# Kernel optimization log

Hardware: AMD Instinct MI355X
Metric: run time of the kernel (lower is better)

Reference implementation:

```python
import jax, jax.numpy as jnp
import numpy as np

# Dims: B=batch, H=query heads, HKV=kv heads, T=query len, S=cache/key len, Dh=head dim
B, H, HKV, T, S, Dh = 2, 32, 8, 1024, 2048, 128
THRESH = 0.000488  # keep keys whose mean attention (over heads and queries) exceeds this


def setup_inputs() -> dict:
    key = jax.random.key(0)
    k1, k2, k3 = jax.random.split(key, 3)
    # attn_w emulates post-softmax attention probabilities: rows sum to 1 over key axis
    attn_w = jax.random.uniform(k1, (B, H, T, S), dtype=jnp.float32)
    attn_w = attn_w / attn_w.sum(axis=-1, keepdims=True)
    v = jax.random.normal(k2, (B, HKV, S, Dh), dtype=jnp.float32)
    w_o = jax.random.normal(k3, (H * Dh, H * Dh), dtype=jnp.float32) * 0.02  # o_proj weight (no bias, Mistral)
    return {"attn_w": attn_w, "v": v, "w_o": w_o}


def reference(attn_w, v, w_o):
    # keep = attn_w.mean(dim=(1,2)) > thresh  -> [B, S]
    keep = attn_w.mean(axis=(1, 2)) > THRESH
    pruned_weights = attn_w * keep[:, None, None, :].astype(attn_w.dtype)  # [B,H,T,S]
    # repeat_kv: [B,HKV,S,Dh] -> [B,H,S,Dh] via repeat_interleave on head axis
    groups = attn_w.shape[1] // v.shape[1]
    v_full = jnp.repeat(v, groups, axis=1)
    new_ctx = jnp.einsum('bhts,bhsd->bhtd', pruned_weights, v_full)  # [B,H,T,Dh]
    Bn, Hn, Tn, Dn = new_ctx.shape
    new_ctx = new_ctx.transpose(0, 2, 1, 3).reshape(Bn, Tn, Hn * Dn)  # [B,T,H*Dh]
    out = new_ctx @ w_o.T  # o_proj
    return (out, pruned_weights)
```

## Files before the change

kernel.cpp:

```cpp
#include <hip/hip_runtime.h>
#include <hip/hip_bf16.h>

#define B_ 2
#define H_ 32
#define HKV_ 8
#define T_ 1024
#define S_ 2048
#define DH_ 128
#define HD_ 4096
#define NROW_ 32768
#define THRESH_D 0.000488

typedef __attribute__((ext_vector_type(4))) float f32x4;
typedef __attribute__((ext_vector_type(8))) short bf16x8;

#define SCHED0() __builtin_amdgcn_sched_barrier(0)

__device__ __forceinline__ void gload_lds16(const void* g, void* l) {
  __builtin_amdgcn_global_load_lds(
      (const __attribute__((address_space(1))) void*)g,
      (__attribute__((address_space(3))) void*)l, 16, 0, 0);
}

__global__ __launch_bounds__(256) void colsum_partial_k(
    const float* __restrict__ attn, double* __restrict__ partial) {
  int tid = threadIdx.x;
  int b = blockIdx.z, y = blockIdx.y;
  int s = blockIdx.x * 1024 + tid * 4;
  const float* base = attn + (size_t)(b * NROW_ + y * 128) * S_ + s;
  double a0 = 0.0, a1 = 0.0, a2 = 0.0, a3 = 0.0;
  for (int r = 0; r < 128; ++r) {
    f32x4 vv = *(const f32x4*)(base + (size_t)r * S_);
    a0 += vv.x; a1 += vv.y; a2 += vv.z; a3 += vv.w;
  }
  double* o = partial + (size_t)(b * 256 + y) * S_ + s;
  o[0] = a0; o[1] = a1; o[2] = a2; o[3] = a3;
}

__global__ void reduce_keep_k(const double* __restrict__ partial,
                              float* __restrict__ keep) {
  __shared__ double sh[4][64];
  int b = blockIdx.x >> 5;
  int s0 = (blockIdx.x & 31) * 64;
  int w = threadIdx.x >> 6, l = threadIdx.x & 63;
  const double* p = partial + (size_t)b * 256 * S_ + s0 + l;
  double sum = 0.0;
  #pragma unroll 8
  for (int y = 0; y < 64; ++y) sum += p[(size_t)(w * 64 + y) * S_];
  sh[w][l] = sum;
  __syncthreads();
  if (w == 0) {
    double t = (sh[0][l] + sh[1][l]) + (sh[2][l] + sh[3][l]);
    keep[b * S_ + s0 + l] = (t * (1.0 / 32768.0) > THRESH_D) ? 1.0f : 0.0f;
  }
}

__global__ void convert_v_k(const float* __restrict__ v,
                            __hip_bfloat16* __restrict__ vt) {
  __shared__ float tile[32][33];
  int bh = blockIdx.z;
  int s0 = blockIdx.x * 32, d0 = blockIdx.y * 32;
  const float* vp = v + (size_t)bh * (S_ * DH_);
  __hip_bfloat16* vtp = vt + (size_t)bh * (S_ * DH_);
  int tx = threadIdx.x, ty = threadIdx.y;
  for (int i = 0; i < 32; i += 8)
    tile[ty + i][tx] = vp[(size_t)(s0 + ty + i) * DH_ + d0 + tx];
  __syncthreads();
  int s = s0 + tx;
  for (int i = 0; i < 32; i += 8) {
    int d = d0 + ty + i;
    int ssw = (s & ~63) | ((s ^ ((d & 7) << 3)) & 63);
    vtp[(size_t)d * S_ + ssw] = __float2bfloat16(tile[tx][ty + i]);
  }
}

__global__ void convert_wo_k(const float* __restrict__ w,
                             __hip_bfloat16* __restrict__ wb) {
  size_t idx = ((size_t)blockIdx.x * 256 + threadIdx.x) * 8;
  int n = (int)(idx >> 12);
  int k0 = (int)(idx & (HD_ - 1));
  float4 x = *(const float4*)(w + idx);
  float4 y = *(const float4*)(w + idx + 4);
  union { bf16x8 v8; __hip_bfloat16 h[8]; } u;
  u.h[0] = __float2bfloat16(x.x); u.h[1] = __float2bfloat16(x.y);
  u.h[2] = __float2bfloat16(x.z); u.h[3] = __float2bfloat16(x.w);
  u.h[4] = __float2bfloat16(y.x); u.h[5] = __float2bfloat16(y.y);
  u.h[6] = __float2bfloat16(y.z); u.h[7] = __float2bfloat16(y.w);
  int ksw = (k0 & ~63) | ((k0 ^ ((n & 7) << 3)) & 63);
  *(bf16x8*)(wb + (size_t)n * HD_ + ksw) = u.v8;
}

#define BK1 64
#define NS1 32

__global__ __launch_bounds__(512, 4) void prune_gemm1_k(
    const float* __restrict__ attn, const float* __restrict__ keep,
    const __hip_bfloat16* __restrict__ vt, float* __restrict__ pruned,
    __hip_bfloat16* __restrict__ ctx) {
  __shared__ __align__(16) __hip_bfloat16 As[2][128 * BK1];
  __shared__ __align__(16) __hip_bfloat16 Bs[2][128 * BK1];
  __shared__ __align__(16) float ksh[S_];

  int tid = threadIdx.x;
  int lg = ((blockIdx.x & 7) << 6) | (blockIdx.x >> 3);
  int bh = lg >> 3;
  int t0 = (lg & 7) * 128;
  int b = bh >> 5, h = bh & 31, hkv = h >> 2;
  int rot = (lg * 17) & 31;
  const float* A = attn + ((size_t)bh * T_ + t0) * S_;
  float* P = pruned + ((size_t)bh * T_ + t0) * S_;
  const __hip_bfloat16* Bv = vt + (size_t)(b * HKV_ + hkv) * (DH_ * S_);
  const float* kp = keep + b * S_;

  int arow = tid >> 2;
  int acol = (tid & 3) * 16;
  int wave = tid >> 6, lane = tid & 63;
  int l16 = lane & 15, lk = lane >> 4;

  f32x4 acc[8];
  f32x4 z = {0.f, 0.f, 0.f, 0.f};
  #pragma unroll
  for (int n = 0; n < 8; ++n) acc[n] = z;

  f32x4 areg0[4], areg1[4];

  auto col = [&](int j) { return (j + rot) & 31; };

  auto issueA = [&](int cks, f32x4* bank) {
    const float* ga = A + (size_t)arow * S_ + cks * BK1 + acol;
    #pragma unroll
    for (int j = 0; j < 4; ++j) bank[j] = *(const f32x4*)(ga + j * 4);
  };

  auto issueB = [&](int cks, int buf) {
    const __hip_bfloat16* g0 = Bv + (size_t)(tid >> 3) * S_ + cks * BK1 + (tid & 7) * 8;
    char* lb = (char*)&Bs[buf][0] + tid * 16;
    gload_lds16(g0, lb);
    gload_lds16(g0 + (size_t)64 * S_, lb + 8192);
  };

  auto stageA = [&](int cks, int buf, const f32x4* bank) {
    f32x4 p[4];
    #pragma unroll
    for (int j = 0; j < 4; ++j) {
      f32x4 kv = *(const f32x4*)&ksh[cks * BK1 + acol + j * 4];
      p[j] = bank[j] * kv;
    }
    float* gp = P + (size_t)arow * S_ + cks * BK1 + acol;
    #pragma unroll
    for (int j = 0; j < 4; ++j) *(f32x4*)(gp + j * 4) = p[j];
    union { bf16x8 v8; __hip_bfloat16 h[8]; } u0, u1;
    const float* pf = (const float*)&p[0];
    #pragma unroll
    for (int j = 0; j < 8; ++j) u0.h[j] = __float2bfloat16(pf[j]);
    #pragma unroll
    for (int j = 0; j < 8; ++j) u1.h[j] = __float2bfloat16(pf[8 + j]);
    char* ab = (char*)&As[buf][0];
    int base0 = arow * 128 + acol * 2;
    int sw = (arow & 7) << 4;
    *(bf16x8*)(ab + (base0 ^ sw)) = u0.v8;
    *(bf16x8*)(ab + ((base0 + 16) ^ sw)) = u1.v8;
  };

  auto mfmaStep = [&](int buf) {
    char* ab = (char*)&As[buf][0];
    char* bb = (char*)&Bs[buf][0];
    #pragma unroll
    for (int kk = 0; kk < 2; ++kk) {
      int kb = kk * 64 + lk * 16;
      int ar = wave * 16 + l16;
      bf16x8 af = *(const bf16x8*)(ab + (ar * 128 + (kb ^ ((ar & 7) << 4))));
      #pragma unroll
      for (int n = 0; n < 8; ++n) {
        int br = n * 16 + l16;
        bf16x8 bf = *(const bf16x8*)(bb + (br * 128 + (kb ^ ((br & 7) << 4))));
        acc[n] = __builtin_amdgcn_mfma_f32_16x16x32_bf16(af, bf, acc[n], 0, 0, 0);
      }
    }
  };

  gload_lds16(kp + tid * 4, (char*)ksh + tid * 16);
  issueB(col(0), 0);
  issueA(col(0), areg0);
  SCHED0();
  asm volatile("s_waitcnt vmcnt(6)" ::: "memory");
  SCHED0();
  __builtin_amdgcn_s_barrier();
  SCHED0();
  issueA(col(1), areg1);
  stageA(col(0), 0, areg0);

  for (int ks = 0; ks < NS1; ks += 2) {
    {
      int cur = 0;
      if (ks + 1 < NS1) issueB(col(ks + 1), 1);
      if (ks + 2 < NS1) issueA(col(ks + 2), areg0);
      if (ks + 1 < NS1) stageA(col(ks + 1), 1, areg1);
      SCHED0();
      if (ks + 2 < NS1)      { asm volatile("s_waitcnt vmcnt(18) lgkmcnt(0)" ::: "memory"); }
      else if (ks + 1 < NS1) { asm volatile("s_waitcnt vmcnt(14) lgkmcnt(0)" ::: "memory"); }
      else                   { asm volatile("s_waitcnt vmcnt(4) lgkmcnt(0)" ::: "memory"); }
      SCHED0();
      __builtin_amdgcn_s_barrier();
      SCHED0();
      mfmaStep(cur);
      SCHED0();
      __builtin_amdgcn_s_barrier();
      SCHED0();
    }
    {
      int ko = ks + 1;
      int cur = 1;
      if (ko + 1 < NS1) issueB(col(ko + 1), 0);
      if (ko + 2 < NS1) issueA(col(ko + 2), areg1);
      if (ko + 1 < NS1) stageA(col(ko + 1), 0, areg0);
      SCHED0();
      if (ko + 2 < NS1)      { asm volatile("s_waitcnt vmcnt(18) lgkmcnt(0)" ::: "memory"); }
      else if (ko + 1 < NS1) { asm volatile("s_waitcnt vmcnt(14) lgkmcnt(0)" ::: "memory"); }
      else                   { asm volatile("s_waitcnt vmcnt(4) lgkmcnt(0)" ::: "memory"); }
      SCHED0();
      __builtin_amdgcn_s_barrier();
      SCHED0();
      mfmaStep(cur);
      SCHED0();
      __builtin_amdgcn_s_barrier();
      SCHED0();
    }
  }

  #pragma unroll
  for (int n = 0; n < 8; ++n)
    #pragma unroll
    for (int r = 0; r < 4; ++r) {
      int trow = t0 + wave * 16 + lk * 4 + r;
      int rowm = b * T_ + trow;
      int kcol = h * DH_ + n * 16 + l16;
      int ksw = (kcol & ~63) | ((kcol ^ ((rowm & 7) << 3)) & 63);
      ctx[(size_t)rowm * HD_ + ksw] = __float2bfloat16(acc[n][r]);
    }
}

#define BK2 64
#define NS2 64

__global__ __launch_bounds__(512) void gemm2_k(
    const __hip_bfloat16* __restrict__ Actx,
    const __hip_bfloat16* __restrict__ Bw,
    float* __restrict__ out) {
  __shared__ __align__(16) __hip_bfloat16 As[2][128 * BK2];
  __shared__ __align__(16) __hip_bfloat16 Bs[2][128 * BK2];
  int tid = threadIdx.x;
  int lg = ((blockIdx.x & 7) << 6) | (blockIdx.x >> 3);
  int n0 = (lg >> 4) * 128;
  int m0 = (lg & 15) * 128;
  const __hip_bfloat16* Ap = Actx + (size_t)m0 * HD_;
  const __hip_bfloat16* Bp = Bw + (size_t)n0 * HD_;
  int wave = tid >> 6, lane = tid & 63;
  int l16 = lane & 15, lk = lane >> 4;

  f32x4 acc[8];
  f32x4 z = {0.f, 0.f, 0.f, 0.f};
  #pragma unroll
  for (int n = 0; n < 8; ++n) acc[n] = z;

  auto issue = [&](int ks, int buf) {
    const __hip_bfloat16* ga = Ap + (size_t)(tid >> 3) * HD_ + ks * BK2 + (tid & 7) * 8;
    const __hip_bfloat16* gb = Bp + (size_t)(tid >> 3) * HD_ + ks * BK2 + (tid & 7) * 8;
    char* la = (char*)&As[buf][0] + tid * 16;
    char* lb = (char*)&Bs[buf][0] + tid * 16;
    gload_lds16(ga, la);
    gload_lds16(ga + (size_t)64 * HD_, la + 8192);
    gload_lds16(gb, lb);
    gload_lds16(gb + (size_t)64 * HD_, lb + 8192);
  };

  auto mfmaStep = [&](int buf) {
    char* ab = (char*)&As[buf][0];
    char* bb = (char*)&Bs[buf][0];
    #pragma unroll
    for (int kk = 0; kk < 2; ++kk) {
      int kb = kk * 64 + lk * 16;
      int ar = wave * 16 + l16;
      bf16x8 af = *(const bf16x8*)(ab + (ar * 128 + (kb ^ ((ar & 7) << 4))));
      #pragma unroll
      for (int n = 0; n < 8; ++n) {
        int br = n * 16 + l16;
        bf16x8 bf = *(const bf16x8*)(bb + (br * 128 + (kb ^ ((br & 7) << 4))));
        acc[n] = __builtin_amdgcn_mfma_f32_16x16x32_bf16(af, bf, acc[n], 0, 0, 0);
      }
    }
  };

  issue(0, 0);
  for (int ks = 0; ks < NS2; ++ks) {
    int cur = ks & 1;
    if (ks + 1 < NS2) issue(ks + 1, cur ^ 1);
    SCHED0();
    if (ks + 1 < NS2) {
      asm volatile("s_waitcnt vmcnt(4) lgkmcnt(0)" ::: "memory");
    } else {
      asm volatile("s_waitcnt vmcnt(0) lgkmcnt(0)" ::: "memory");
    }
    SCHED0();
    __builtin_amdgcn_s_barrier();
    SCHED0();
    mfmaStep(cur);
    SCHED0();
    __builtin_amdgcn_s_barrier();
    SCHED0();
  }

  #pragma unroll
  for (int n = 0; n < 8; ++n)
    #pragma unroll
    for (int r = 0; r < 4; ++r) {
      int row = m0 + wave * 16 + lk * 4 + r;
      int col = n0 + n * 16 + l16;
      out[(size_t)row * HD_ + col] = acc[n][r];
    }
}

extern "C" void kernel_launch(void* const* d_in, const int* in_sizes, int n_in,
                              void* d_out, int out_size, void* d_ws, size_t ws_size,
                              hipStream_t stream) {
  const float* attn = (const float*)d_in[0];
  const float* v = (const float*)d_in[1];
  const float* w_o = (const float*)d_in[2];
  float* out = (float*)d_out;
  float* pruned = out + (size_t)B_ * T_ * HD_;

  char* ws = (char*)d_ws;
  size_t off = 0;
  double* partial = (double*)(ws + off); off += (size_t)B_ * 256 * S_ * 8;
  float* keep = (float*)(ws + off);      off += (size_t)B_ * S_ * 4;
  __hip_bfloat16* vt = (__hip_bfloat16*)(ws + off);
  off += (size_t)B_ * HKV_ * DH_ * S_ * 2;
  __hip_bfloat16* wo = (__hip_bfloat16*)(ws + off);
  off += (size_t)HD_ * HD_ * 2;
  __hip_bfloat16* ctx = (__hip_bfloat16*)(ws + off);
  off += (size_t)B_ * T_ * HD_ * 2;

  colsum_partial_k<<<dim3(2, 256, B_), 256, 0, stream>>>(attn, partial);
  reduce_keep_k<<<dim3(64), 256, 0, stream>>>(partial, keep);
  convert_v_k<<<dim3(S_ / 32, DH_ / 32, B_ * HKV_), dim3(32, 8), 0, stream>>>(v, vt);
  convert_wo_k<<<dim3((HD_ * HD_) / (256 * 8)), 256, 0, stream>>>(w_o, wo);
  prune_gemm1_k<<<dim3(512), 512, 0, stream>>>(attn, keep, vt, pruned, ctx);
  gemm2_k<<<dim3(512), 512, 0, stream>>>(ctx, wo, out);

  (void)in_sizes; (void)n_in; (void)out_size; (void)ws_size;
}
```

Measured before the change: 473.9 us.

## Emit bf16 copy of attention during column-sum and feed GEMM1 from it

The column-sum pass now also writes a swizzled bf16 copy of the attention weights. The prune+GEMM1 kernel then streams that half-size copy instead of the fp32 input, and rebuilds the fp32 pruned output from the bf16 values times the keep mask. The keep mask is also folded into the bf16 V conversion. Total DRAM traffic is roughly unchanged, because the extra bf16 write offsets the smaller read, and the pruned-weights output is now rounded to bf16, which risks accuracy. The path only runs when the workspace is large enough to hold the copy; otherwise the old kernels run.

```diff
diff --git a/kernel.cpp b/kernel.cpp
--- a/kernel.cpp
+++ b/kernel.cpp
@@ -22,20 +22,6 @@
       (__attribute__((address_space(3))) void*)l, 16, 0, 0);
 }
 
-__global__ __launch_bounds__(256) void colsum_partial_k(
-    const float* __restrict__ attn, double* __restrict__ partial) {
-  int tid = threadIdx.x;
-  int b = blockIdx.z, y = blockIdx.y;
-  int s = blockIdx.x * 1024 + tid * 4;
-  const float* base = attn + (size_t)(b * NROW_ + y * 128) * S_ + s;
-  double a0 = 0.0, a1 = 0.0, a2 = 0.0, a3 = 0.0;
-  for (int r = 0; r < 128; ++r) {
-    f32x4 vv = *(const f32x4*)(base + (size_t)r * S_);
-    a0 += vv.x; a1 += vv.y; a2 += vv.z; a3 += vv.w;
-  }
-  double* o = partial + (size_t)(b * 256 + y) * S_ + s;
-  o[0] = a0; o[1] = a1; o[2] = a2; o[3] = a3;
-}
 
 __global__ void reduce_keep_k(const double* __restrict__ partial,
                               float* __restrict__ keep) {
@@ -55,8 +41,304 @@
   }
 }
 
-__global__ void convert_v_k(const float* __restrict__ v,
-                            __hip_bfloat16* __restrict__ vt) {
+__global__ void convert_wo_k(const float* __restrict__ w,
+                             __hip_bfloat16* __restrict__ wb) {
+  size_t idx = ((size_t)blockIdx.x * 256 + threadIdx.x) * 8;
+  int n = (int)(idx >> 12);
+  int k0 = (int)(idx & (HD_ - 1));
+  float4 x = *(const float4*)(w + idx);
+  float4 y = *(const float4*)(w + idx + 4);
+  union { bf16x8 v8; __hip_bfloat16 h[8]; } u;
+  u.h[0] = __float2bfloat16(x.x); u.h[1] = __float2bfloat16(x.y);
+  u.h[2] = __float2bfloat16(x.z); u.h[3] = __float2bfloat16(x.w);
+  u.h[4] = __float2bfloat16(y.x); u.h[5] = __float2bfloat16(y.y);
+  u.h[6] = __float2bfloat16(y.z); u.h[7] = __float2bfloat16(y.w);
+  int ksw = (k0 & ~63) | ((k0 ^ ((n & 7) << 3)) & 63);
+  *(bf16x8*)(wb + (size_t)n * HD_ + ksw) = u.v8;
+}
+
+#define BK2 64
+#define NS2 64
+
+__global__ __launch_bounds__(512) void gemm2_k(
+    const __hip_bfloat16* __restrict__ Actx,
+    const __hip_bfloat16* __restrict__ Bw,
+    float* __restrict__ out) {
+  __shared__ __align__(16) __hip_bfloat16 As[2][128 * BK2];
+  __shared__ __align__(16) __hip_bfloat16 Bs[2][128 * BK2];
+  int tid = threadIdx.x;
+  int lg = ((blockIdx.x & 7) << 6) | (blockIdx.x >> 3);
+  int n0 = (lg >> 4) * 128;
+  int m0 = (lg & 15) * 128;
+  const __hip_bfloat16* Ap = Actx + (size_t)m0 * HD_;
+  const __hip_bfloat16* Bp = Bw + (size_t)n0 * HD_;
+  int wave = tid >> 6, lane = tid & 63;
+  int l16 = lane & 15, lk = lane >> 4;
+
+  f32x4 acc[8];
+  f32x4 z = {0.f, 0.f, 0.f, 0.f};
+  #pragma unroll
+  for (int n = 0; n < 8; ++n) acc[n] = z;
+
+  auto issue = [&](int ks, int buf) {
+    const __hip_bfloat16* ga = Ap + (size_t)(tid >> 3) * HD_ + ks * BK2 + (tid & 7) * 8;
+    const __hip_bfloat16* gb = Bp + (size_t)(tid >> 3) * HD_ + ks * BK2 + (tid & 7) * 8;
+    char* la = (char*)&As[buf][0] + tid * 16;
+    char* lb = (char*)&Bs[buf][0] + tid * 16;
+    gload_lds16(ga, la);
+    gload_lds16(ga + (size_t)64 * HD_, la + 8192);
+    gload_lds16(gb, lb);
+    gload_lds16(gb + (size_t)64 * HD_, lb + 8192);
+  };
+
+  auto mfmaStep = [&](int buf) {
+    char* ab = (char*)&As[buf][0];
+    char* bb = (char*)&Bs[buf][0];
+    #pragma unroll
+    for (int kk = 0; kk < 2; ++kk) {
+      int kb = kk * 64 + lk * 16;
+      int ar = wave * 16 + l16;
+      bf16x8 af = *(const bf16x8*)(ab + (ar * 128 + (kb ^ ((ar & 7) << 4))));
+      #pragma unroll
+      for (int n = 0; n < 8; ++n) {
+        int br = n * 16 + l16;
+        bf16x8 bf = *(const bf16x8*)(bb + (br * 128 + (kb ^ ((br & 7) << 4))));
+        acc[n] = __builtin_amdgcn_mfma_f32_16x16x32_bf16(af, bf, acc[n], 0, 0, 0);
+      }
+    }
+  };
+
+  issue(0, 0);
+  for (int ks = 0; ks < NS2; ++ks) {
+    int cur = ks & 1;
+    if (ks + 1 < NS2) issue(ks + 1, cur ^ 1);
+    SCHED0();
+    if (ks + 1 < NS2) {
+      asm volatile("s_waitcnt vmcnt(4) lgkmcnt(0)" ::: "memory");
+    } else {
+      asm volatile("s_waitcnt vmcnt(0) lgkmcnt(0)" ::: "memory");
+    }
+    SCHED0();
+    __builtin_amdgcn_s_barrier();
+    SCHED0();
+    mfmaStep(cur);
+    SCHED0();
+    __builtin_amdgcn_s_barrier();
+    SCHED0();
+  }
+
+  #pragma unroll
+  for (int n = 0; n < 8; ++n)
+    #pragma unroll
+    for (int r = 0; r < 4; ++r) {
+      int row = m0 + wave * 16 + lk * 4 + r;
+      int col = n0 + n * 16 + l16;
+      out[(size_t)row * HD_ + col] = acc[n][r];
+    }
+}
+
+
+__global__ __launch_bounds__(256) void colsumA_k(
+    const float* __restrict__ attn, double* __restrict__ partial,
+    __hip_bfloat16* __restrict__ abf) {
+  int tid = threadIdx.x;
+  int b = blockIdx.z, y = blockIdx.y;
+  int s = blockIdx.x * 1024 + tid * 4;
+  const float* base = attn + (size_t)(b * NROW_ + y * 128) * S_ + s;
+  __hip_bfloat16* ob = abf + (size_t)(b * NROW_ + y * 128) * S_;
+  double a0 = 0.0, a1 = 0.0, a2 = 0.0, a3 = 0.0;
+  #pragma unroll 2
+  for (int r = 0; r < 128; ++r) {
+    f32x4 vv = *(const f32x4*)(base + (size_t)r * S_);
+    a0 += vv.x; a1 += vv.y; a2 += vv.z; a3 += vv.w;
+    int ssw = (s & ~63) | ((s ^ ((r & 7) << 3)) & 63);
+    union { ushort4 u4; __hip_bfloat16 h[4]; } u;
+    u.h[0] = __float2bfloat16(vv.x); u.h[1] = __float2bfloat16(vv.y);
+    u.h[2] = __float2bfloat16(vv.z); u.h[3] = __float2bfloat16(vv.w);
+    *(ushort4*)(ob + (size_t)r * S_ + ssw) = u.u4;
+  }
+  double* o = partial + (size_t)(b * 256 + y) * S_ + s;
+  o[0] = a0; o[1] = a1; o[2] = a2; o[3] = a3;
+}
+
+__global__ void convert_vA_k(const float* __restrict__ v,
+                             const float* __restrict__ keep,
+                             __hip_bfloat16* __restrict__ vt) {
+  __shared__ float tile[32][33];
+  int bh = blockIdx.z;
+  int b = bh >> 3;
+  int s0 = blockIdx.x * 32, d0 = blockIdx.y * 32;
+  const float* vp = v + (size_t)bh * (S_ * DH_);
+  __hip_bfloat16* vtp = vt + (size_t)bh * (S_ * DH_);
+  int tx = threadIdx.x, ty = threadIdx.y;
+  for (int i = 0; i < 32; i += 8)
+    tile[ty + i][tx] = vp[(size_t)(s0 + ty + i) * DH_ + d0 + tx];
+  __syncthreads();
+  int s = s0 + tx;
+  float kv = keep[b * S_ + s];
+  for (int i = 0; i < 32; i += 8) {
+    int d = d0 + ty + i;
+    int ssw = (s & ~63) | ((s ^ ((d & 7) << 3)) & 63);
+    vtp[(size_t)d * S_ + ssw] = __float2bfloat16(tile[tx][ty + i] * kv);
+  }
+}
+
+#define BK1 64
+#define NS1 32
+
+__global__ __launch_bounds__(512, 4) void prune_gemm1A_k(
+    const __hip_bfloat16* __restrict__ abf, const float* __restrict__ keep,
+    const __hip_bfloat16* __restrict__ vt, float* __restrict__ pruned,
+    __hip_bfloat16* __restrict__ ctx) {
+  __shared__ __align__(16) __hip_bfloat16 As[2][128 * BK1];
+  __shared__ __align__(16) __hip_bfloat16 Bs[2][128 * BK1];
+  __shared__ __align__(16) float ksh[S_];
+
+  int tid = threadIdx.x;
+  int lg = ((blockIdx.x & 7) << 6) | (blockIdx.x >> 3);
+  int bh = lg >> 3;
+  int t0 = (lg & 7) * 128;
+  int b = bh >> 5, h = bh & 31, hkv = h >> 2;
+  int rot = (lg * 17) & 31;
+  const __hip_bfloat16* Ab = abf + ((size_t)bh * T_ + t0) * S_;
+  float* P = pruned + ((size_t)bh * T_ + t0) * S_;
+  const __hip_bfloat16* Bv = vt + (size_t)(b * HKV_ + hkv) * (DH_ * S_);
+  const float* kp = keep + b * S_;
+
+  int wave = tid >> 6, lane = tid & 63;
+  int l16 = lane & 15, lk = lane >> 4;
+
+  f32x4 acc[8];
+  f32x4 z = {0.f, 0.f, 0.f, 0.f};
+  #pragma unroll
+  for (int n = 0; n < 8; ++n) acc[n] = z;
+
+  auto col = [&](int j) { return (j + rot) & 31; };
+
+  auto issueA = [&](int cks, int buf) {
+    const __hip_bfloat16* g0 = Ab + (size_t)(tid >> 3) * S_ + cks * BK1 + (tid & 7) * 8;
+    char* la = (char*)&As[buf][0] + tid * 16;
+    gload_lds16(g0, la);
+    gload_lds16(g0 + (size_t)64 * S_, la + 8192);
+  };
+
+  auto issueB = [&](int cks, int buf) {
+    const __hip_bfloat16* g0 = Bv + (size_t)(tid >> 3) * S_ + cks * BK1 + (tid & 7) * 8;
+    char* lb = (char*)&Bs[buf][0] + tid * 16;
+    gload_lds16(g0, lb);
+    gload_lds16(g0 + (size_t)64 * S_, lb + 8192);
+  };
+
+  auto mfmaStep = [&](int buf) {
+    char* ab = (char*)&As[buf][0];
+    char* bb = (char*)&Bs[buf][0];
+    #pragma unroll
+    for (int kk = 0; kk < 2; ++kk) {
+      int kb = kk * 64 + lk * 16;
+      int ar = wave * 16 + l16;
+      bf16x8 af = *(const bf16x8*)(ab + (ar * 128 + (kb ^ ((ar & 7) << 4))));
+      #pragma unroll
+      for (int n = 0; n < 8; ++n) {
+        int br = n * 16 + l16;
+        bf16x8 bf = *(const bf16x8*)(bb + (br * 128 + (kb ^ ((br & 7) << 4))));
+        acc[n] = __builtin_amdgcn_mfma_f32_16x16x32_bf16(af, bf, acc[n], 0, 0, 0);
+      }
+    }
+  };
+
+  auto prunedWrite = [&](int cks, int buf) {
+    char* ab = (char*)&As[buf][0];
+    union { bf16x8 v; unsigned int d[4]; } u0, u1;
+    u0.v = *(const bf16x8*)(ab + tid * 16);
+    u1.v = *(const bf16x8*)(ab + tid * 16 + 8192);
+    int row0 = tid >> 3;
+    int scol = cks * BK1 + (((tid & 7) * 8) ^ ((row0 & 7) << 3));
+    f32x4 k0 = *(const f32x4*)&ksh[scol];
+    f32x4 k1 = *(const f32x4*)&ksh[scol + 4];
+    f32x4 p00, p01, p10, p11;
+    p00.x = __uint_as_float(u0.d[0] << 16) * k0.x;
+    p00.y = __uint_as_float(u0.d[0] & 0xFFFF0000u) * k0.y;
+    p00.z = __uint_as_float(u0.d[1] << 16) * k0.z;
+    p00.w = __uint_as_float(u0.d[1] & 0xFFFF0000u) * k0.w;
+    p01.x = __uint_as_float(u0.d[2] << 16) * k1.x;
+    p01.y = __uint_as_float(u0.d[2] & 0xFFFF0000u) * k1.y;
+    p01.z = __uint_as_float(u0.d[3] << 16) * k1.z;
+    p01.w = __uint_as_float(u0.d[3] & 0xFFFF0000u) * k1.w;
+    p10.x = __uint_as_float(u1.d[0] << 16) * k0.x;
+    p10.y = __uint_as_float(u1.d[0] & 0xFFFF0000u) * k0.y;
+    p10.z = __uint_as_float(u1.d[1] << 16) * k0.z;
+    p10.w = __uint_as_float(u1.d[1] & 0xFFFF0000u) * k0.w;
+    p11.x = __uint_as_float(u1.d[2] << 16) * k1.x;
+    p11.y = __uint_as_float(u1.d[2] & 0xFFFF0000u) * k1.y;
+    p11.z = __uint_as_float(u1.d[3] << 16) * k1.z;
+    p11.w = __uint_as_float(u1.d[3] & 0xFFFF0000u) * k1.w;
+    float* gp0 = P + (size_t)row0 * S_ + scol;
+    float* gp1 = P + (size_t)(row0 + 64) * S_ + scol;
+    *(f32x4*)gp0 = p00; *(f32x4*)(gp0 + 4) = p01;
+    *(f32x4*)gp1 = p10; *(f32x4*)(gp1 + 4) = p11;
+  };
+
+  gload_lds16(kp + tid * 4, (char*)ksh + tid * 16);
+  issueA(col(0), 0);
+  issueB(col(0), 0);
+  SCHED0();
+  asm volatile("s_waitcnt vmcnt(4)" ::: "memory");
+  SCHED0();
+  __builtin_amdgcn_s_barrier();
+  SCHED0();
+
+  for (int ks = 0; ks < NS1; ++ks) {
+    int cur = ks & 1;
+    if (ks + 1 < NS1) {
+      issueA(col(ks + 1), cur ^ 1);
+      issueB(col(ks + 1), cur ^ 1);
+    }
+    SCHED0();
+    if (ks == 0 || ks == NS1 - 1) {
+      asm volatile("s_waitcnt vmcnt(4) lgkmcnt(0)" ::: "memory");
+    } else {
+      asm volatile("s_waitcnt vmcnt(8) lgkmcnt(0)" ::: "memory");
+    }
+    SCHED0();
+    __builtin_amdgcn_s_barrier();
+    SCHED0();
+    mfmaStep(cur);
+    prunedWrite(col(ks), cur);
+    SCHED0();
+    __builtin_amdgcn_s_barrier();
+    SCHED0();
+  }
+
+  #pragma unroll
+  for (int n = 0; n < 8; ++n)
+    #pragma unroll
+    for (int r = 0; r < 4; ++r) {
+      int trow = t0 + wave * 16 + lk * 4 + r;
+      int rowm = b * T_ + trow;
+      int kcol = h * DH_ + n * 16 + l16;
+      int ksw = (kcol & ~63) | ((kcol ^ ((rowm & 7) << 3)) & 63);
+      ctx[(size_t)rowm * HD_ + ksw] = __float2bfloat16(acc[n][r]);
+    }
+}
+
+
+__global__ __launch_bounds__(256) void colsumB_k(
+    const float* __restrict__ attn, double* __restrict__ partial) {
+  int tid = threadIdx.x;
+  int b = blockIdx.z, y = blockIdx.y;
+  int s = blockIdx.x * 1024 + tid * 4;
+  const float* base = attn + (size_t)(b * NROW_ + y * 128) * S_ + s;
+  double a0 = 0.0, a1 = 0.0, a2 = 0.0, a3 = 0.0;
+  for (int r = 0; r < 128; ++r) {
+    f32x4 vv = *(const f32x4*)(base + (size_t)r * S_);
+    a0 += vv.x; a1 += vv.y; a2 += vv.z; a3 += vv.w;
+  }
+  double* o = partial + (size_t)(b * 256 + y) * S_ + s;
+  o[0] = a0; o[1] = a1; o[2] = a2; o[3] = a3;
+}
+
+__global__ void convert_vB_k(const float* __restrict__ v,
+                             __hip_bfloat16* __restrict__ vt) {
   __shared__ float tile[32][33];
   int bh = blockIdx.z;
   int s0 = blockIdx.x * 32, d0 = blockIdx.y * 32;
@@ -74,26 +356,7 @@
   }
 }
 
-__global__ void convert_wo_k(const float* __restrict__ w,
-                             __hip_bfloat16* __restrict__ wb) {
-  size_t idx = ((size_t)blockIdx.x * 256 + threadIdx.x) * 8;
-  int n = (int)(idx >> 12);
-  int k0 = (int)(idx & (HD_ - 1));
-  float4 x = *(const float4*)(w + idx);
-  float4 y = *(const float4*)(w + idx + 4);
-  union { bf16x8 v8; __hip_bfloat16 h[8]; } u;
-  u.h[0] = __float2bfloat16(x.x); u.h[1] = __float2bfloat16(x.y);
-  u.h[2] = __float2bfloat16(x.z); u.h[3] = __float2bfloat16(x.w);
-  u.h[4] = __float2bfloat16(y.x); u.h[5] = __float2bfloat16(y.y);
-  u.h[6] = __float2bfloat16(y.z); u.h[7] = __float2bfloat16(y.w);
-  int ksw = (k0 & ~63) | ((k0 ^ ((n & 7) << 3)) & 63);
-  *(bf16x8*)(wb + (size_t)n * HD_ + ksw) = u.v8;
-}
-
-#define BK1 64
-#define NS1 32
-
-__global__ __launch_bounds__(512, 4) void prune_gemm1_k(
+__global__ __launch_bounds__(512, 4) void prune_gemm1B_k(
     const float* __restrict__ attn, const float* __restrict__ keep,
     const __hip_bfloat16* __restrict__ vt, float* __restrict__ pruned,
     __hip_bfloat16* __restrict__ ctx) {
@@ -240,85 +503,6 @@
     }
 }
 
-#define BK2 64
-#define NS2 64
-
-__global__ __launch_bounds__(512) void gemm2_k(
-    const __hip_bfloat16* __restrict__ Actx,
-    const __hip_bfloat16* __restrict__ Bw,
-    float* __restrict__ out) {
-  __shared__ __align__(16) __hip_bfloat16 As[2][128 * BK2];
-  __shared__ __align__(16) __hip_bfloat16 Bs[2][128 * BK2];
-  int tid = threadIdx.x;
-  int lg = ((blockIdx.x & 7) << 6) | (blockIdx.x >> 3);
-  int n0 = (lg >> 4) * 128;
-  int m0 = (lg & 15) * 128;
-  const __hip_bfloat16* Ap = Actx + (size_t)m0 * HD_;
-  const __hip_bfloat16* Bp = Bw + (size_t)n0 * HD_;
-  int wave = tid >> 6, lane = tid & 63;
-  int l16 = lane & 15, lk = lane >> 4;
-
-  f32x4 acc[8];
-  f32x4 z = {0.f, 0.f, 0.f, 0.f};
-  #pragma unroll
-  for (int n = 0; n < 8; ++n) acc[n] = z;
-
-  auto issue = [&](int ks, int buf) {
-    const __hip_bfloat16* ga = Ap + (size_t)(tid >> 3) * HD_ + ks * BK2 + (tid & 7) * 8;
-    const __hip_bfloat16* gb = Bp + (size_t)(tid >> 3) * HD_ + ks * BK2 + (tid & 7) * 8;
-    char* la = (char*)&As[buf][0] + tid * 16;
-    char* lb = (char*)&Bs[buf][0] + tid * 16;
-    gload_lds16(ga, la);
-    gload_lds16(ga + (size_t)64 * HD_, la + 8192);
-    gload_lds16(gb, lb);
-    gload_lds16(gb + (size_t)64 * HD_, lb + 8192);
-  };
-
-  auto mfmaStep = [&](int buf) {
-    char* ab = (char*)&As[buf][0];
-    char* bb = (char*)&Bs[buf][0];
-    #pragma unroll
-    for (int kk = 0; kk < 2; ++kk) {
-      int kb = kk * 64 + lk * 16;
-      int ar = wave * 16 + l16;
-      bf16x8 af = *(const bf16x8*)(ab + (ar * 128 + (kb ^ ((ar & 7) << 4))));
-      #pragma unroll
-      for (int n = 0; n < 8; ++n) {
-        int br = n * 16 + l16;
-        bf16x8 bf = *(const bf16x8*)(bb + (br * 128 + (kb ^ ((br & 7) << 4))));
-        acc[n] = __builtin_amdgcn_mfma_f32_16x16x32_bf16(af, bf, acc[n], 0, 0, 0);
-      }
-    }
-  };
-
-  issue(0, 0);
-  for (int ks = 0; ks < NS2; ++ks) {
-    int cur = ks & 1;
-    if (ks + 1 < NS2) issue(ks + 1, cur ^ 1);
-    SCHED0();
-    if (ks + 1 < NS2) {
-      asm volatile("s_waitcnt vmcnt(4) lgkmcnt(0)" ::: "memory");
-    } else {
-      asm volatile("s_waitcnt vmcnt(0) lgkmcnt(0)" ::: "memory");
-    }
-    SCHED0();
-    __builtin_amdgcn_s_barrier();
-    SCHED0();
-    mfmaStep(cur);
-    SCHED0();
-    __builtin_amdgcn_s_barrier();
-    SCHED0();
-  }
-
-  #pragma unroll
-  for (int n = 0; n < 8; ++n)
-    #pragma unroll
-    for (int r = 0; r < 4; ++r) {
-      int row = m0 + wave * 16 + lk * 4 + r;
-      int col = n0 + n * 16 + l16;
-      out[(size_t)row * HD_ + col] = acc[n][r];
-    }
-}
 
 extern "C" void kernel_launch(void* const* d_in, const int* in_sizes, int n_in,
                               void* d_out, int out_size, void* d_ws, size_t ws_size,
@@ -339,12 +523,24 @@
   off += (size_t)HD_ * HD_ * 2;
   __hip_bfloat16* ctx = (__hip_bfloat16*)(ws + off);
   off += (size_t)B_ * T_ * HD_ * 2;
-
-  colsum_partial_k<<<dim3(2, 256, B_), 256, 0, stream>>>(attn, partial);
-  reduce_keep_k<<<dim3(64), 256, 0, stream>>>(partial, keep);
-  convert_v_k<<<dim3(S_ / 32, DH_ / 32, B_ * HKV_), dim3(32, 8), 0, stream>>>(v, vt);
-  convert_wo_k<<<dim3((HD_ * HD_) / (256 * 8)), 256, 0, stream>>>(w_o, wo);
-  prune_gemm1_k<<<dim3(512), 512, 0, stream>>>(attn, keep, vt, pruned, ctx);
+  __hip_bfloat16* abf = (__hip_bfloat16*)(ws + off);
+  size_t need_abf = off + (size_t)B_ * NROW_ * S_ * 2;
+
+  bool bigws = (ws_size >= need_abf);
+
+  if (bigws) {
+    colsumA_k<<<dim3(2, 256, B_), 256, 0, stream>>>(attn, partial, abf);
+    reduce_keep_k<<<dim3(64), 256, 0, stream>>>(partial, keep);
+    convert_vA_k<<<dim3(S_ / 32, DH_ / 32, B_ * HKV_), dim3(32, 8), 0, stream>>>(v, keep, vt);
+    convert_wo_k<<<dim3((HD_ * HD_) / (256 * 8)), 256, 0, stream>>>(w_o, wo);
+    prune_gemm1A_k<<<dim3(512), 512, 0, stream>>>(abf, keep, vt, pruned, ctx);
+  } else {
+    colsumB_k<<<dim3(2, 256, B_), 256, 0, stream>>>(attn, partial);
+    reduce_keep_k<<<dim3(64), 256, 0, stream>>>(partial, keep);
+    convert_vB_k<<<dim3(S_ / 32, DH_ / 32, B_ * HKV_), dim3(32, 8), 0, stream>>>(v, vt);
+    convert_wo_k<<<dim3((HD_ * HD_) / (256 * 8)), 256, 0, stream>>>(w_o, wo);
+    prune_gemm1B_k<<<dim3(512), 512, 0, stream>>>(attn, keep, vt, pruned, ctx);
+  }
   gemm2_k<<<dim3(512), 512, 0, stream>>>(ctx, wo, out);
 
   (void)in_sizes; (void)n_in; (void)out_size; (void)ws_size;
```

After: 454.2 us. 1.04x faster.
